# Kernel optimization log

Hardware: AMD Instinct MI355X
Metric: run time of the kernel (lower is better)

Reference implementation:

```python
import jax, jax.numpy as jnp
import numpy as np

B, S, D_IN, D_OUT, H = 4, 2048, 1024, 1024, 16
HD = D_OUT // H

def setup_inputs() -> dict:
    key = jax.random.key(0)
    ks = jax.random.split(key, 6)
    s = 1.0 / np.sqrt(D_IN)
    return {
        "x": jax.random.normal(ks[0], (B, S, D_IN), dtype=jnp.float32),
        "Wq": jax.random.uniform(ks[1], (D_IN, D_OUT), jnp.float32, -s, s),
        "Wk": jax.random.uniform(ks[2], (D_IN, D_OUT), jnp.float32, -s, s),
        "Wv": jax.random.uniform(ks[3], (D_IN, D_OUT), jnp.float32, -s, s),
        "Wo": jax.random.uniform(ks[4], (D_OUT, D_OUT), jnp.float32, -s, s),
        "bo": jax.random.uniform(ks[5], (D_OUT,), jnp.float32, -s, s),
    }

def reference(x, Wq, Wk, Wv, Wo, bo):
    b, n, _ = x.shape
    # project and split heads: [b, h, n, hd]
    q = (x @ Wq).reshape(b, n, H, HD).transpose(0, 2, 1, 3)
    k = (x @ Wk).reshape(b, n, H, HD).transpose(0, 2, 1, 3)
    v = (x @ Wv).reshape(b, n, H, HD).transpose(0, 2, 1, 3)
    scores = jnp.einsum("bhqd,bhkd->bhqk", q, k) / np.sqrt(HD).astype(np.float32)
    causal = jnp.tril(jnp.ones((n, n), dtype=bool))
    scores = jnp.where(causal, scores, -jnp.inf)
    attn = jax.nn.softmax(scores, axis=-1)  # dropout p=0.0 -> identity
    ctx = jnp.einsum("bhqk,bhkd->bhqd", attn, v)
    ctx = ctx.transpose(0, 2, 1, 3).reshape(b, n, D_OUT)
    return ctx @ Wo + bo
```

## Files before the change

### kernel.cpp

```cpp
#include <hip/hip_runtime.h>
#include <stdint.h>

#define B_   4
#define S_   2048
#define DI   1024
#define DOUT 1024
#define NHD  16
#define HD   64

typedef __attribute__((ext_vector_type(8))) short short8;
typedef __attribute__((ext_vector_type(4))) float f32x4;
typedef __attribute__((ext_vector_type(16))) float f32x16;

__device__ __forceinline__ unsigned short f32_bf16(float f) {
  union { float f; unsigned u; } v; v.f = f;
  unsigned r = v.u + 0x7FFFu + ((v.u >> 16) & 1u);
  return (unsigned short)(r >> 16);
}

__device__ __forceinline__ unsigned cvt_pk_bf16(float a, float b) {
  unsigned r;
  asm("v_cvt_pk_bf16_f32 %0, %1, %2" : "=v"(r) : "v"(a), "v"(b));
  return r;
}

__device__ __forceinline__ void pl32swap(unsigned &dst, unsigned &src) {
  asm("v_permlane32_swap_b32 %0, %1" : "+v"(dst), "+v"(src));
}

__device__ __forceinline__ float max3f(float a, float b, float c) {
  float d;
  asm("v_max3_f32 %0, %1, %2, %3" : "=v"(d) : "v"(a), "v"(b), "v"(c));
  return d;
}

__device__ __forceinline__ void gl_lds16(const void* g, void* s) {
  __builtin_amdgcn_global_load_lds(
      (const __attribute__((address_space(1))) unsigned int*)g,
      (__attribute__((address_space(3))) unsigned int*)s, 16, 0, 0);
}

#define EXP2(x) __builtin_amdgcn_exp2f(x)

__global__ __launch_bounds__(256) void cvt_kernel(const float* __restrict__ src,
                                                  unsigned short* __restrict__ dst, int n4) {
  int i = blockIdx.x * blockDim.x + threadIdx.x;
  if (i < n4) {
    float4 v = ((const float4*)src)[i];
    ushort4 o;
    o.x = f32_bf16(v.x); o.y = f32_bf16(v.y); o.z = f32_bf16(v.z); o.w = f32_bf16(v.w);
    ((ushort4*)dst)[i] = o;
  }
}

__global__ __launch_bounds__(256) void wtrans4_kernel(
    const float* __restrict__ W0, const float* __restrict__ W1,
    const float* __restrict__ W2, const float* __restrict__ W3,
    unsigned short* __restrict__ T0, unsigned short* __restrict__ T1,
    unsigned short* __restrict__ T2, unsigned short* __restrict__ T3) {
  __shared__ __attribute__((aligned(16))) float tile[64][65];
  const int z = blockIdx.z;
  const float* W = z == 0 ? W0 : z == 1 ? W1 : z == 2 ? W2 : W3;
  unsigned short* Wt = z == 0 ? T0 : z == 1 ? T1 : z == 2 ? T2 : T3;
  const int k0 = blockIdx.y * 64;
  const int n0 = blockIdx.x * 64;
  const int tid = threadIdx.x;
#pragma unroll
  for (int i = 0; i < 4; i++) {
    int c = tid + i * 256;
    int r = c >> 4;
    int cc = (c & 15) * 4;
    float4 v = *(const float4*)(W + (size_t)(k0 + r) * DOUT + n0 + cc);
    tile[r][cc] = v.x; tile[r][cc + 1] = v.y; tile[r][cc + 2] = v.z; tile[r][cc + 3] = v.w;
  }
  __syncthreads();
#pragma unroll
  for (int i = 0; i < 4; i++) {
    int c = tid + i * 256;
    int r = c >> 4;
    int cc = (c & 15) * 4;
    ushort4 o;
    o.x = f32_bf16(tile[cc + 0][r]);
    o.y = f32_bf16(tile[cc + 1][r]);
    o.z = f32_bf16(tile[cc + 2][r]);
    o.w = f32_bf16(tile[cc + 3][r]);
    *(ushort4*)(Wt + (size_t)(n0 + r) * DI + k0 + cc) = o;
  }
}

__device__ __forceinline__ int cswz(int r, int c) {
  return r * 128 + ((((c >> 3) ^ ((r >> 3) & 15)) << 3) | (c & 7));
}

template <int MODE>
__global__ __launch_bounds__(256) void gemm_kernel(
    const unsigned short* __restrict__ A,
    const unsigned short* __restrict__ Bt,
    unsigned short* __restrict__ oQ,
    unsigned short* __restrict__ oK,
    unsigned short* __restrict__ oV,
    float* __restrict__ outF,
    const float* __restrict__ bias,
    int M, int N, int K) {
  __shared__ __attribute__((aligned(16))) unsigned short smem[16384];
  const int tid = threadIdx.x;
  const int lane = tid & 63;
  const int w = tid >> 6;
  const int wm = w >> 1, wn = w & 1;
  const int quad = lane >> 4, l16 = lane & 15;

  const int bid = blockIdx.y * 64 + blockIdx.x;
  const int xcd = bid & 7;
  const int rr = bid >> 3;
  const int bx = xcd * 8 + (rr & 7);
  const int by = rr >> 3;
  const int m0 = bx * 128;
  const int n0 = by * 128;

  const int lr = lane >> 2;
  const int lc8 = (lane & 3) * 8;
  const unsigned short* gA0 = A + (size_t)(m0 + w * 32 + lr) * K + lc8;
  const unsigned short* gA1 = gA0 + (size_t)16 * K;
  const unsigned short* gB0 = Bt + (size_t)(n0 + w * 32 + lr) * K + lc8;
  const unsigned short* gB1 = gB0 + (size_t)16 * K;
  const int sA0o = (w * 2 + 0) * 512;
  const int sA1o = (w * 2 + 1) * 512;
  const int sB0o = 4096 + (w * 2 + 0) * 512;
  const int sB1o = 4096 + (w * 2 + 1) * 512;

  f32x4 acc[4][4] = {};

  gl_lds16(gA0, smem + sA0o);
  gl_lds16(gA1, smem + sA1o);
  gl_lds16(gB0, smem + sB0o);
  gl_lds16(gB1, smem + sB1o);
  __syncthreads();

  for (int k0 = 0; k0 < K; k0 += 32) {
    const int cb = ((k0 >> 5) & 1) << 13;
    const int nb = 8192 - cb;
    if (k0 + 32 < K) {
      gl_lds16(gA0 + k0 + 32, smem + nb + sA0o);
      gl_lds16(gA1 + k0 + 32, smem + nb + sA1o);
      gl_lds16(gB0 + k0 + 32, smem + nb + sB0o);
      gl_lds16(gB1 + k0 + 32, smem + nb + sB1o);
    }
    short8 af[4], bfr[4];
#pragma unroll
    for (int mi = 0; mi < 4; mi++)
      af[mi] = *(const short8*)(smem + cb + (wm * 64 + mi * 16 + l16) * 32 + quad * 8);
#pragma unroll
    for (int ni = 0; ni < 4; ni++)
      bfr[ni] = *(const short8*)(smem + cb + 4096 + (wn * 64 + ni * 16 + l16) * 32 + quad * 8);
#pragma unroll
    for (int mi = 0; mi < 4; mi++)
#pragma unroll
      for (int ni = 0; ni < 4; ni++)
        acc[mi][ni] = __builtin_amdgcn_mfma_f32_16x16x32_bf16(af[mi], bfr[ni], acc[mi][ni], 0, 0, 0);
    __syncthreads();
  }

  if (MODE == 0) {
    const int which = n0 >> 10;
    if (which == 2) {
#pragma unroll
      for (int mi = 0; mi < 4; mi++)
#pragma unroll
        for (int ni = 0; ni < 4; ni++)
#pragma unroll
          for (int r = 0; r < 4; r++)
            smem[cswz(wm * 64 + mi * 16 + quad * 4 + r, wn * 64 + ni * 16 + l16)] =
                f32_bf16(acc[mi][ni][r]);
      __syncthreads();
      const int b = m0 >> 11, sb = m0 & 2047;
#pragma unroll
      for (int i = 0; i < 8; i++) {
        int c = tid + i * 256;
        int cl = c >> 4;
        int sc = (c & 15) * 8;
        int col = n0 + cl;
        int hh = (col >> 6) & 15, hd = col & 63;
        union { unsigned short u[8]; uint4 v; } t;
#pragma unroll
        for (int jx = 0; jx < 8; jx++) t.u[jx] = smem[cswz(sc + jx, cl)];
        *(uint4*)(oV + (((size_t)(b * NHD + hh)) * HD + hd) * S_ + sb + sc) = t.v;
      }
    } else {
      unsigned short* dst0 = which == 0 ? oQ : oK;
#pragma unroll
      for (int mi = 0; mi < 4; mi++)
#pragma unroll
        for (int ni = 0; ni < 4; ni++) {
          const int col = n0 + wn * 64 + ni * 16 + l16;
          const int hh = (col >> 6) & 15, hd = col & 63;
#pragma unroll
          for (int r = 0; r < 4; r++) {
            const int row = m0 + wm * 64 + mi * 16 + quad * 4 + r;
            int b = row >> 11, s = row & 2047;
            dst0[(((size_t)(b * NHD + hh)) * S_ + s) * HD + hd] = f32_bf16(acc[mi][ni][r]);
          }
        }
    }
  } else {
#pragma unroll
    for (int mi = 0; mi < 4; mi++)
#pragma unroll
      for (int ni = 0; ni < 4; ni++) {
        const int col = n0 + wn * 64 + ni * 16 + l16;
        float bv = bias[col];
#pragma unroll
        for (int r = 0; r < 4; r++) {
          const int row = m0 + wm * 64 + mi * 16 + quad * 4 + r;
          outF[(size_t)row * N + col] = acc[mi][ni][r] + bv;
        }
      }
  }
}

__global__ __launch_bounds__(256, 4) void attn_kernel(
    const unsigned short* __restrict__ Q,
    const unsigned short* __restrict__ Kmat,
    const unsigned short* __restrict__ Vt,
    unsigned short* __restrict__ ctx) {
  __shared__ __attribute__((aligned(16))) unsigned short smem[16384];

  const int tid = threadIdx.x;
  const int lane = tid & 63;
  const int w = tid >> 6;
  const int l32 = lane & 31;
  const int h = lane >> 5;

  const int bid = blockIdx.x;
  const int bh = (bid & 7) * 8 + ((bid >> 3) & 7);
  const int jj = bid >> 6;

  const unsigned short* Qh = Q + (size_t)bh * S_ * HD;
  const unsigned short* Kh = Kmat + (size_t)bh * S_ * HD;
  const unsigned short* Vh = Vt + (size_t)bh * HD * S_;

  const int sr = tid >> 2;
  const int jA = tid & 3, jB = jA + 4;
  const int sswA = sr * 64 + ((jA ^ (sr & 7)) << 3);
  const int sswB = sr * 64 + ((jB ^ (sr & 7)) << 3);
  const unsigned short* gKA = Kh + (size_t)sr * HD + jA * 8;
  const unsigned short* gKB = Kh + (size_t)sr * HD + jB * 8;
  const unsigned short* gVA = Vh + (size_t)sr * S_ + jA * 8;
  const unsigned short* gVB = Vh + (size_t)sr * S_ + jB * 8;
  const int swz = (l32 & 7);

  unsigned short* myP = smem + (size_t)(w * 32) * 72;
  const float scl = 0.18033688f;
  const int b = bh >> 4, head = bh & 15;

  for (int ph = 0; ph < 2; ph++) {
    const int qc = (ph == 0) ? (jj * 8 + w) : (63 - jj * 8 - w);
    const int nt = (qc >> 1) + 1;
    const int ntmax = (ph == 0) ? (jj * 4 + 2) : (32 - jj * 4);
    const int qrow = qc * 32 + l32;

    short8 qf[4];
#pragma unroll
    for (int ks = 0; ks < 4; ks++)
      qf[ks] = *(const short8*)(Qh + (size_t)qrow * HD + ks * 16 + h * 8);

    uint4 kregA = *(const uint4*)gKA, kregB = *(const uint4*)gKB;
    uint4 vregA = *(const uint4*)gVA, vregB = *(const uint4*)gVB;
    *(uint4*)(smem + sswA) = kregA;
    *(uint4*)(smem + sswB) = kregB;
    *(uint4*)(smem + 8192 + sswA) = vregA;
    *(uint4*)(smem + 8192 + sswB) = vregB;
    __syncthreads();

    f32x16 oacc[2] = {};
    float m_run = -__builtin_inff();
    float l_run = 0.f;

    for (int kt = 0; kt < ntmax; kt++) {
      if (kt + 1 < ntmax) {
        kregA = *(const uint4*)(gKA + (size_t)(kt + 1) * 64 * HD);
        kregB = *(const uint4*)(gKB + (size_t)(kt + 1) * 64 * HD);
        vregA = *(const uint4*)(gVA + (size_t)(kt + 1) * 64);
        vregB = *(const uint4*)(gVB + (size_t)(kt + 1) * 64);
      }
      const unsigned short* Kb_ = smem + ((kt & 1) << 12);
      const unsigned short* Vb_ = smem + 8192 + ((kt & 1) << 12);

      if (kt < nt) {
        const int k0 = kt * 64;
        f32x16 sacc[2] = {};
#pragma unroll
        for (int ks = 0; ks < 4; ks++)
#pragma unroll
          for (int mi = 0; mi < 2; mi++) {
            short8 kf = *(const short8*)(Kb_ + (mi * 32 + l32) * 64 + (((ks * 2 + h) ^ swz) << 3));
            sacc[mi] = __builtin_amdgcn_mfma_f32_32x32x16_bf16(kf, qf[ks], sacc[mi], 0, 0, 0);
          }

        if (kt == nt - 1) {
#pragma unroll
          for (int mi = 0; mi < 2; mi++)
#pragma unroll
            for (int e = 0; e < 16; e++) {
              int key = k0 + mi * 32 + (e & 3) + 8 * (e >> 2) + 4 * h;
              if (key > qrow) sacc[mi][e] = -__builtin_inff();
            }
        }
        float vmax = fmaxf(sacc[0][0], sacc[0][1]);
#pragma unroll
        for (int e = 2; e < 16; e += 2) vmax = max3f(vmax, sacc[0][e], sacc[0][e + 1]);
#pragma unroll
        for (int e = 0; e < 16; e += 2) vmax = max3f(vmax, sacc[1][e], sacc[1][e + 1]);
        vmax = fmaxf(vmax, __shfl_xor(vmax, 32));
        const float pm = vmax * scl;
        if (!__all(pm <= m_run + 8.f)) {
          const float mnew = fmaxf(m_run, pm);
          const float alpha = EXP2(m_run - mnew);
          m_run = mnew;
          l_run *= alpha;
#pragma unroll
          for (int mi = 0; mi < 2; mi++) oacc[mi] *= alpha;
        }

        float rs = 0.f;
#pragma unroll
        for (int mi = 0; mi < 2; mi++)
#pragma unroll
          for (int e = 0; e < 16; e++) {
            float p = EXP2(fmaf(sacc[mi][e], scl, -m_run));
            sacc[mi][e] = p;
            rs += p;
          }
        rs += __shfl_xor(rs, 32);
        l_run += rs;

        short8 pfr[4];
#pragma unroll
        for (int mi = 0; mi < 2; mi++) {
          unsigned w0 = cvt_pk_bf16(sacc[mi][0], sacc[mi][1]);
          unsigned w1 = cvt_pk_bf16(sacc[mi][2], sacc[mi][3]);
          unsigned w2 = cvt_pk_bf16(sacc[mi][4], sacc[mi][5]);
          unsigned w3 = cvt_pk_bf16(sacc[mi][6], sacc[mi][7]);
          pl32swap(w0, w2);
          pl32swap(w1, w3);
          union { unsigned u[4]; short8 s; } lo;
          lo.u[0] = w0; lo.u[1] = w1; lo.u[2] = w2; lo.u[3] = w3;
          pfr[2 * mi + 0] = lo.s;
          unsigned x0 = cvt_pk_bf16(sacc[mi][8], sacc[mi][9]);
          unsigned x1 = cvt_pk_bf16(sacc[mi][10], sacc[mi][11]);
          unsigned x2 = cvt_pk_bf16(sacc[mi][12], sacc[mi][13]);
          unsigned x3 = cvt_pk_bf16(sacc[mi][14], sacc[mi][15]);
          pl32swap(x0, x2);
          pl32swap(x1, x3);
          union { unsigned u[4]; short8 s; } hi;
          hi.u[0] = x0; hi.u[1] = x1; hi.u[2] = x2; hi.u[3] = x3;
          pfr[2 * mi + 1] = hi.s;
        }

#pragma unroll
        for (int ks2 = 0; ks2 < 4; ks2++) {
#pragma unroll
          for (int mi2 = 0; mi2 < 2; mi2++) {
            short8 vf = *(const short8*)(Vb_ + (mi2 * 32 + l32) * 64 + (((ks2 * 2 + h) ^ swz) << 3));
            oacc[mi2] = __builtin_amdgcn_mfma_f32_32x32x16_bf16(vf, pfr[ks2], oacc[mi2], 0, 0, 0);
          }
        }
      }

      if (kt + 1 < ntmax) {
        *(uint4*)(smem + ((~kt & 1) << 12) + sswA) = kregA;
        *(uint4*)(smem + ((~kt & 1) << 12) + sswB) = kregB;
        *(uint4*)(smem + 8192 + ((~kt & 1) << 12) + sswA) = vregA;
        *(uint4*)(smem + 8192 + ((~kt & 1) << 12) + sswB) = vregB;
      }
      __syncthreads();
    }

    const float inv = 1.f / l_run;
#pragma unroll
    for (int mi2 = 0; mi2 < 2; mi2++)
#pragma unroll
      for (int g = 0; g < 4; g++) {
        uint2 pk;
        pk.x = cvt_pk_bf16(oacc[mi2][4 * g + 0] * inv, oacc[mi2][4 * g + 1] * inv);
        pk.y = cvt_pk_bf16(oacc[mi2][4 * g + 2] * inv, oacc[mi2][4 * g + 3] * inv);
        *(uint2*)(myP + l32 * 72 + mi2 * 32 + g * 8 + h * 4) = pk;
      }
#pragma unroll
    for (int p = 0; p < 4; p++) {
      int r = p * 8 + (lane >> 3);
      int c = (lane & 7) * 8;
      uint4 vv = *(const uint4*)(myP + r * 72 + c);
      *(uint4*)(ctx + ((size_t)(b * S_ + qc * 32 + r)) * DOUT + head * 64 + c) = vv;
    }
    __syncthreads();
  }
}

extern "C" void kernel_launch(void* const* d_in, const int* in_sizes, int n_in,
                              void* d_out, int out_size, void* d_ws, size_t ws_size,
                              hipStream_t stream) {
  const float* x  = (const float*)d_in[0];
  const float* Wq = (const float*)d_in[1];
  const float* Wk = (const float*)d_in[2];
  const float* Wv = (const float*)d_in[3];
  const float* Wo = (const float*)d_in[4];
  const float* bo = (const float*)d_in[5];
  float* out = (float*)d_out;
  char* ws = (char*)d_ws;

  const size_t MB = 1024 * 1024;
  unsigned short* Wqt = (unsigned short*)(ws + 0 * MB);
  unsigned short* Wkt = (unsigned short*)(ws + 2 * MB);
  unsigned short* Wvt = (unsigned short*)(ws + 4 * MB);
  unsigned short* Wot = (unsigned short*)(ws + 6 * MB);
  unsigned short* xb  = (unsigned short*)(ws + 8 * MB);
  unsigned short* Qb  = (unsigned short*)(ws + 24 * MB);
  unsigned short* Kb  = (unsigned short*)(ws + 40 * MB);
  unsigned short* Vtb = (unsigned short*)(ws + 72 * MB);
  unsigned short* ctxb = xb;

  cvt_kernel<<<8192, 256, 0, stream>>>(x, xb, 2097152);
  wtrans4_kernel<<<dim3(16, 16, 4), 256, 0, stream>>>(Wq, Wk, Wv, Wo, Wqt, Wkt, Wvt, Wot);
  gemm_kernel<0><<<dim3(64, 24), 256, 0, stream>>>(xb, Wqt, Qb, Kb, Vtb, nullptr, nullptr,
                                                   8192, 3072, 1024);
  attn_kernel<<<512, 256, 0, stream>>>(Qb, Kb, Vtb, ctxb);
  gemm_kernel<1><<<dim3(64, 8), 256, 0, stream>>>(ctxb, Wot, nullptr, nullptr, nullptr, out, bo,
                                                  8192, 1024, 1024);
}
```

Baseline: 260.1 us.

## Stage attention K/V tiles with direct global-to-LDS loads instead of register staging

Replaces the register-staged double-buffered K/V prefetch in the attention kernel with direct global-to-LDS 16-byte loads (gl_lds16), with the swizzle moved to the global source address. This removes the VGPRs that held the prefetched tiles and the explicit LDS store instructions. Launch bounds are relaxed from 4 to 2 blocks per CU, which allows more registers per thread but may lower occupancy. It relies on a gl_lds16 helper defined elsewhere and on the async LDS writes finishing before the barrier.

```diff
diff --git a/kernel.cpp b/kernel.cpp
--- a/kernel.cpp
+++ b/kernel.cpp
@@ -217,7 +217,7 @@
   }
 }
 
-__global__ __launch_bounds__(256, 4) void attn_kernel(
+__global__ __launch_bounds__(256, 2) void attn_kernel(
     const unsigned short* __restrict__ Q,
     const unsigned short* __restrict__ Kmat,
     const unsigned short* __restrict__ Vt,
@@ -238,19 +238,25 @@
   const unsigned short* Kh = Kmat + (size_t)bh * S_ * HD;
   const unsigned short* Vh = Vt + (size_t)bh * HD * S_;
 
-  const int sr = tid >> 2;
-  const int jA = tid & 3, jB = jA + 4;
-  const int sswA = sr * 64 + ((jA ^ (sr & 7)) << 3);
-  const int sswB = sr * 64 + ((jB ^ (sr & 7)) << 3);
-  const unsigned short* gKA = Kh + (size_t)sr * HD + jA * 8;
-  const unsigned short* gKB = Kh + (size_t)sr * HD + jB * 8;
-  const unsigned short* gVA = Vh + (size_t)sr * S_ + jA * 8;
-  const unsigned short* gVB = Vh + (size_t)sr * S_ + jB * 8;
+  const int r1 = tid >> 3, c1 = tid & 7;
+  const int sj1 = c1 ^ (r1 & 7);
+  const unsigned short* gK1 = Kh + (size_t)r1 * HD + sj1 * 8;
+  const unsigned short* gV1 = Vh + (size_t)r1 * S_ + sj1 * 8;
   const int swz = (l32 & 7);
 
   unsigned short* myP = smem + (size_t)(w * 32) * 72;
   const float scl = 0.18033688f;
   const int b = bh >> 4, head = bh & 15;
+
+#define ASTAGE(t, bf)                                                       \
+  do {                                                                      \
+    const unsigned short* k_ = gK1 + (size_t)(t) * 64 * HD;                 \
+    const unsigned short* v_ = gV1 + (size_t)(t) * 64;                      \
+    gl_lds16(k_, smem + (bf) * 4096 + w * 512);                             \
+    gl_lds16(k_ + 32 * HD, smem + (bf) * 4096 + 2048 + w * 512);            \
+    gl_lds16(v_, smem + 8192 + (bf) * 4096 + w * 512);                      \
+    gl_lds16(v_ + (size_t)32 * S_, smem + 8192 + (bf) * 4096 + 2048 + w * 512); \
+  } while (0)
 
   for (int ph = 0; ph < 2; ph++) {
     const int qc = (ph == 0) ? (jj * 8 + w) : (63 - jj * 8 - w);
@@ -263,12 +269,7 @@
     for (int ks = 0; ks < 4; ks++)
       qf[ks] = *(const short8*)(Qh + (size_t)qrow * HD + ks * 16 + h * 8);
 
-    uint4 kregA = *(const uint4*)gKA, kregB = *(const uint4*)gKB;
-    uint4 vregA = *(const uint4*)gVA, vregB = *(const uint4*)gVB;
-    *(uint4*)(smem + sswA) = kregA;
-    *(uint4*)(smem + sswB) = kregB;
-    *(uint4*)(smem + 8192 + sswA) = vregA;
-    *(uint4*)(smem + 8192 + sswB) = vregB;
+    ASTAGE(0, 0);
     __syncthreads();
 
     f32x16 oacc[2] = {};
@@ -276,12 +277,8 @@
     float l_run = 0.f;
 
     for (int kt = 0; kt < ntmax; kt++) {
-      if (kt + 1 < ntmax) {
-        kregA = *(const uint4*)(gKA + (size_t)(kt + 1) * 64 * HD);
-        kregB = *(const uint4*)(gKB + (size_t)(kt + 1) * 64 * HD);
-        vregA = *(const uint4*)(gVA + (size_t)(kt + 1) * 64);
-        vregB = *(const uint4*)(gVB + (size_t)(kt + 1) * 64);
-      }
+      if (kt + 1 < ntmax) ASTAGE(kt + 1, (kt + 1) & 1);
+
       const unsigned short* Kb_ = smem + ((kt & 1) << 12);
       const unsigned short* Vb_ = smem + 8192 + ((kt & 1) << 12);
 
@@ -366,12 +363,6 @@
         }
       }
 
-      if (kt + 1 < ntmax) {
-        *(uint4*)(smem + ((~kt & 1) << 12) + sswA) = kregA;
-        *(uint4*)(smem + ((~kt & 1) << 12) + sswB) = kregB;
-        *(uint4*)(smem + 8192 + ((~kt & 1) << 12) + sswA) = vregA;
-        *(uint4*)(smem + 8192 + ((~kt & 1) << 12) + sswB) = vregB;
-      }
       __syncthreads();
     }
 
@@ -394,6 +385,7 @@
     }
     __syncthreads();
   }
+#undef ASTAGE
 }
 
 extern "C" void kernel_launch(void* const* d_in, const int* in_sizes, int n_in,
```

Result: faster. 236.1 us (-9.2%).
